# Optimization experiments

Hardware: AMD Instinct MI355X
Metric: run time of the kernel (lower is better)

Reference implementation:

```python
import jax, jax.numpy as jnp
import numpy as np

N, D_IN, D_EMB, K = 16384, 1024, 256, 1024
ALPHA, EPS = 0.01, 1e-5


def setup_inputs() -> dict:
    key = jax.random.key(0)
    ks = jax.random.split(key, 6)
    inp = jax.random.normal(ks[0], (N, D_IN), dtype=jnp.float32)
    W_send = jax.random.normal(ks[1], (D_IN, D_EMB), dtype=jnp.float32) / np.sqrt(D_IN)
    b_send = jnp.zeros((D_EMB,), dtype=jnp.float32)
    W_recv = jax.random.normal(ks[2], (D_EMB, D_IN), dtype=jnp.float32) / np.sqrt(D_EMB)
    b_recv = jnp.zeros((D_IN,), dtype=jnp.float32)
    codebook = jax.random.normal(ks[3], (K, D_EMB), dtype=jnp.float32)
    ema_vecs = codebook.copy()
    ema_size = jnp.zeros((K,), dtype=jnp.float32)
    return {"input": inp, "W_send": W_send, "b_send": b_send,
            "W_recv": W_recv, "b_recv": b_recv, "codebook": codebook,
            "ema_vecs": ema_vecs, "ema_size": ema_size}


def reference(input, W_send, b_send, W_recv, b_recv, codebook, ema_vecs, ema_size):
    sg = jax.lax.stop_gradient
    # send projection -> latent z  [N, D_EMB]
    z = input @ W_send + b_send
    # nearest-neighbor lookup: argmin_k ||e_k||^2 - 2 <z, e_k>
    sqr = jnp.sum(codebook * codebook, axis=1)          # [K]
    cov = jnp.einsum('nj,kj->nk', z, codebook)          # [N, K]
    codes = jnp.argmin(sqr - 2.0 * cov, axis=-1)        # [N] int
    # fetch embeddings (gather)
    vectors = codebook[codes]                            # [N, D_EMB]
    # mse losses, reduction='sum'
    embedding = jnp.sum((vectors - sg(z)) ** 2)
    commitment = jnp.sum((z - sg(vectors)) ** 2)
    # straight-through output
    emb_out = z + sg(vectors - z)
    # EMA accumulate (one-hot scatter == segment_sum)
    upd_vecs = jax.ops.segment_sum(z, codes, num_segments=K)              # [K, D_EMB]
    upd_size = jax.ops.segment_sum(jnp.ones((z.shape[0],), z.dtype), codes, num_segments=K)
    ema_vecs_new = ema_vecs + ALPHA * (upd_vecs - ema_vecs)
    ema_size_new = ema_size + ALPHA * (upd_size - ema_size)
    # EMA update (Laplace-smoothed centroid)
    n = jnp.sum(ema_size_new)
    coef = n / (n + K * EPS)
    size = coef * (ema_size_new + EPS)
    weight_new = ema_vecs_new / size[:, None]
    # empirical entropy of the codes in bits
    prob = jnp.bincount(codes, length=K).astype(jnp.float32) / codes.size
    ent = -jnp.sum(jnp.where(prob > 0, prob * jnp.log(prob), 0.0)) / jnp.log(2.0)
    # recv projection
    x = emb_out @ W_recv + b_recv
    return (x, codes, embedding, commitment, ent, ema_vecs_new, ema_size_new, weight_new)
```

## Files before the change

### kernel.cpp

```cpp
#include <hip/hip_runtime.h>
#include <math.h>

#define NROWS 16384
#define DIN   1024
#define DEMB  256
#define KC    1024
#define ALPHA 0.01f
#define EPSV  1e-5f
#define INV2048 4.8828125e-4f
#define CHUNK 32
#define COV_CHUNKS 8

typedef _Float16 f16;
typedef __attribute__((ext_vector_type(4)))  _Float16 f16x4;
typedef __attribute__((ext_vector_type(8)))  _Float16 f16x8;
typedef __attribute__((ext_vector_type(16))) float    f32x16;
typedef unsigned long long u64;

#define OFF_Z       0
#define OFF_R       4194304
#define OFF_SQR     5242880
#define OFF_ZH      5243904
#define OFF_ZL      7341056
#define OFF_WTH     9438208
#define OFF_WTL     9569280
#define OFF_CBH     9700352
#define OFF_CBL     9831424
#define OFF_KEYS    9962496
#define OFF_CODES   9995264
#define OFF_LIST    10011648
#define OFF_OFFS    10028032
#define OFF_UPD     10029056
#define OFF_HIST    10291200
#define OFF_CURSOR  10292224
#define OFF_LOSS    10293248
#define ZERO_LEN    264208
#define OFF_COUNTSF 10293264
#define OFF_SIZE    10294288

#define OUT_X      0
#define OUT_CODES  16777216
#define OUT_EMB    16793600
#define OUT_COMMIT 16793601
#define OUT_ENT    16793602
#define OUT_EMAV   16793603
#define OUT_EMAS   17055747
#define OUT_W      17056771

__device__ __forceinline__ void split_f32(float x, f16& h, f16& l) {
    h = (f16)x;
    l = (f16)((x - (float)h) * 2048.0f);
}

__global__ __launch_bounds__(64) void sqr_kernel(const float* __restrict__ cb,
                                                 float* __restrict__ sqr) {
    int k = blockIdx.x;
    int lane = threadIdx.x;
    float4 v = ((const float4*)cb)[k * 64 + lane];
    float s = v.x * v.x + v.y * v.y + v.z * v.z + v.w * v.w;
    for (int off = 32; off > 0; off >>= 1) s += __shfl_down(s, off, 64);
    if (lane == 0) sqr[k] = s;
}

__global__ __launch_bounds__(256) void split_wt_kernel(const float* __restrict__ W,
                                                       f16* __restrict__ wth,
                                                       f16* __restrict__ wtl) {
    int n = blockIdx.x;
    int t = threadIdx.x;
    f16x4 h4, l4;
#pragma unroll
    for (int j = 0; j < 4; ++j) {
        int k = t * 4 + j;
        float x = W[(size_t)k * DEMB + n];
        f16 h, l; split_f32(x, h, l);
        h4[j] = h; l4[j] = l;
    }
    *(f16x4*)&wth[(size_t)n * DIN + t * 4] = h4;
    *(f16x4*)&wtl[(size_t)n * DIN + t * 4] = l4;
}

__global__ __launch_bounds__(256) void split_cb_kernel(const float* __restrict__ cb,
                                                       f16* __restrict__ cbh,
                                                       f16* __restrict__ cbl) {
    int idx = (blockIdx.x * 256 + threadIdx.x) * 4;
    float4 v = *(const float4*)&cb[idx];
    f16x4 h4, l4;
    f16 h, l;
    split_f32(v.x, h, l); h4[0] = h; l4[0] = l;
    split_f32(v.y, h, l); h4[1] = h; l4[1] = l;
    split_f32(v.z, h, l); h4[2] = h; l4[2] = l;
    split_f32(v.w, h, l); h4[3] = h; l4[3] = l;
    *(f16x4*)&cbh[idx] = h4;
    *(f16x4*)&cbl[idx] = l4;
}

__global__ __launch_bounds__(128) void gemm1_mfma(const float* __restrict__ in,
                                                  const f16* __restrict__ wth,
                                                  const f16* __restrict__ wtl,
                                                  const float* __restrict__ bsend,
                                                  float* __restrict__ z,
                                                  f16* __restrict__ zh,
                                                  f16* __restrict__ zl) {
    __shared__ f16 sAh[64 * 72], sAl[64 * 72];
    __shared__ f16 sBh[128 * 72], sBl[128 * 72];
    const int tid = threadIdx.x;
    const int wave = tid >> 6, lane = tid & 63;
    const int half = lane >> 5, l31 = lane & 31;
    const int rowBase = blockIdx.y * 64;
    const int colBase = blockIdx.x * 128;

    f32x16 accm[2][2] = {};
    f32x16 accx[2][2] = {};

    const int ar = tid >> 1;
    const int ak = (tid & 1) * 32;

    for (int ks = 0; ks < DIN; ks += 64) {
        __syncthreads();
#pragma unroll
        for (int i = 0; i < 8; ++i) {
            float4 v = *(const float4*)&in[(size_t)(rowBase + ar) * DIN + ks + ak + i * 4];
            f16x4 h4, l4; f16 h, l;
            split_f32(v.x, h, l); h4[0] = h; l4[0] = l;
            split_f32(v.y, h, l); h4[1] = h; l4[1] = l;
            split_f32(v.z, h, l); h4[2] = h; l4[2] = l;
            split_f32(v.w, h, l); h4[3] = h; l4[3] = l;
            *(f16x4*)&sAh[ar * 72 + ak + i * 4] = h4;
            *(f16x4*)&sAl[ar * 72 + ak + i * 4] = l4;
        }
#pragma unroll
        for (int i = 0; i < 8; ++i) {
            f16x8 bh = *(const f16x8*)&wth[(size_t)(colBase + tid) * DIN + ks + i * 8];
            f16x8 bl = *(const f16x8*)&wtl[(size_t)(colBase + tid) * DIN + ks + i * 8];
            *(f16x8*)&sBh[tid * 72 + i * 8] = bh;
            *(f16x8*)&sBl[tid * 72 + i * 8] = bl;
        }
        __syncthreads();
#pragma unroll
        for (int t4 = 0; t4 < 4; ++t4) {
            int seg = t4 * 2 + half;
            f16x8 a_h[2], a_l[2], b_h[2], b_l[2];
#pragma unroll
            for (int rt = 0; rt < 2; ++rt) {
                a_h[rt] = *(const f16x8*)&sAh[(rt * 32 + l31) * 72 + seg * 8];
                a_l[rt] = *(const f16x8*)&sAl[(rt * 32 + l31) * 72 + seg * 8];
            }
#pragma unroll
            for (int ct = 0; ct < 2; ++ct) {
                int nl = wave * 64 + ct * 32 + l31;
                b_h[ct] = *(const f16x8*)&sBh[nl * 72 + seg * 8];
                b_l[ct] = *(const f16x8*)&sBl[nl * 72 + seg * 8];
            }
#pragma unroll
            for (int rt = 0; rt < 2; ++rt)
#pragma unroll
                for (int ct = 0; ct < 2; ++ct) {
                    accm[rt][ct] = __builtin_amdgcn_mfma_f32_32x32x16_f16(
                        a_h[rt], b_h[ct], accm[rt][ct], 0, 0, 0);
                    accx[rt][ct] = __builtin_amdgcn_mfma_f32_32x32x16_f16(
                        a_h[rt], b_l[ct], accx[rt][ct], 0, 0, 0);
                    accx[rt][ct] = __builtin_amdgcn_mfma_f32_32x32x16_f16(
                        a_l[rt], b_h[ct], accx[rt][ct], 0, 0, 0);
                }
        }
    }

#pragma unroll
    for (int rt = 0; rt < 2; ++rt)
#pragma unroll
        for (int ct = 0; ct < 2; ++ct) {
            int col = colBase + wave * 64 + ct * 32 + l31;
            float bb = bsend[col];
#pragma unroll
            for (int reg = 0; reg < 16; ++reg) {
                int row = rowBase + rt * 32 + (reg & 3) + 8 * (reg >> 2) + 4 * half;
                float zv = accm[rt][ct][reg] + INV2048 * accx[rt][ct][reg] + bb;
                size_t o = (size_t)row * DEMB + col;
                z[o] = zv;
                f16 h = (f16)zv;
                zh[o] = h;
                zl[o] = (f16)((zv - (float)h) * 2048.0f);
            }
        }
}

__device__ __forceinline__ void cov_stage(const f16* __restrict__ cbh,
                                          const f16* __restrict__ cbl,
                                          f16* sC, int buf, int codeBase,
                                          int wave, int lane) {
#pragma unroll
    for (int i = 0; i < 8; ++i) {
        const int seg = wave * 8 + i;
        const int hl  = seg >> 4;
        const int rp  = seg & 15;
        const int r   = rp * 2 + (lane >> 5);
        const f16* src = (hl ? cbl : cbh)
                       + (size_t)(codeBase + r) * DEMB
                       + (((lane & 31) ^ r) << 3);
        f16* dst = sC + (((buf << 1) + hl) * 32 + rp * 2) * DEMB;
        __builtin_amdgcn_global_load_lds(
            (const __attribute__((address_space(1))) void*)src,
            (__attribute__((address_space(3))) void*)dst,
            16, 0, 0);
    }
}

__global__ __launch_bounds__(256, 2) void cov_mfma_kernel(const f16* __restrict__ zh,
                                                          const f16* __restrict__ zl,
                                                          const f16* __restrict__ cbh,
                                                          const f16* __restrict__ cbl,
                                                          const float* __restrict__ sqr,
                                                          u64* __restrict__ keys) {
    __shared__ f16 sC[2 * 2 * 32 * DEMB];
    const int tid = threadIdx.x;
    const int wave = tid >> 6, lane = tid & 63;
    const int half = lane >> 5, l31 = lane & 31;
    const int rowBase = blockIdx.y * 128 + wave * 32;
    const int myRow = rowBase + l31;
    const int cb0 = blockIdx.x * (COV_CHUNKS * 32);

    cov_stage(cbh, cbl, sC, 0, cb0, wave, lane);

    f16x8 a_h[16], a_l[16];
#pragma unroll
    for (int t = 0; t < 16; ++t) {
        size_t o = (size_t)myRow * DEMB + t * 16 + half * 8;
        a_h[t] = *(const f16x8*)&zh[o];
        a_l[t] = *(const f16x8*)&zl[o];
    }

    float runv[16];
    int   runc[16];
#pragma unroll
    for (int r = 0; r < 16; ++r) { runv[r] = 3.4e38f; runc[r] = 0; }

    for (int cc = 0; cc < COV_CHUNKS; ++cc) {
        __syncthreads();
        if (cc + 1 < COV_CHUNKS)
            cov_stage(cbh, cbl, sC, (cc + 1) & 1, cb0 + (cc + 1) * 32, wave, lane);

        const f16* Ch = sC + ((cc & 1) * 2 + 0) * 32 * DEMB;
        const f16* Cl = sC + ((cc & 1) * 2 + 1) * 32 * DEMB;

        f32x16 accm = {};
        f32x16 accx = {};
#pragma unroll
        for (int t = 0; t < 16; ++t) {
            const int seg = t * 2 + half;
            const int p = ((seg ^ l31) << 3);
            f16x8 b_h = *(const f16x8*)&Ch[l31 * DEMB + p];
            f16x8 b_l = *(const f16x8*)&Cl[l31 * DEMB + p];
            accm = __builtin_amdgcn_mfma_f32_32x32x16_f16(a_h[t], b_h, accm, 0, 0, 0);
            accx = __builtin_amdgcn_mfma_f32_32x32x16_f16(a_h[t], b_l, accx, 0, 0, 0);
            accx = __builtin_amdgcn_mfma_f32_32x32x16_f16(a_l[t], b_h, accx, 0, 0, 0);
        }

        const int code = cb0 + cc * 32 + l31;
        const float sqv = sqr[code];
#pragma unroll
        for (int r = 0; r < 16; ++r) {
            float s = sqv - 2.0f * (accm[r] + INV2048 * accx[r]);
            if (s < runv[r]) { runv[r] = s; runc[r] = code; }
        }
    }

#pragma unroll
    for (int r = 0; r < 16; ++r) {
        float v = runv[r]; int ci = runc[r];
        for (int off = 16; off > 0; off >>= 1) {
            float ov = __shfl_down(v, off, 32);
            int   oc = __shfl_down(ci, off, 32);
            if (ov < v || (ov == v && oc < ci)) { v = ov; ci = oc; }
        }
        if (l31 == 0) {
            int row = rowBase + (r & 3) + 8 * (r >> 2) + 4 * half;
            unsigned ub = __float_as_uint(v);
            ub = (ub & 0x80000000u) ? ~ub : (ub | 0x80000000u);
            u64 key = ((u64)ub << 32) | (unsigned)ci;
            atomicMin(&keys[row], key);
        }
    }
}

__global__ __launch_bounds__(256) void decode_kernel(const u64* __restrict__ keys,
                                                     int* __restrict__ codes,
                                                     float* __restrict__ out_codes,
                                                     int* __restrict__ hist) {
    int r = blockIdx.x * 256 + threadIdx.x;
    int c = (int)(keys[r] & 0xFFFFFFFFull);
    codes[r] = c;
    out_codes[r] = (float)c;
    atomicAdd(&hist[c], 1);
}

__global__ __launch_bounds__(1024) void prefix_kernel(const int* __restrict__ hist,
                                                      int* __restrict__ offs,
                                                      float* __restrict__ countsf) {
    __shared__ int s[1024];
    int t = threadIdx.x;
    int v = hist[t];
    s[t] = v;
    countsf[t] = (float)v;
    __syncthreads();
    for (int d = 1; d < 1024; d <<= 1) {
        int x = (t >= d) ? s[t - d] : 0;
        __syncthreads();
        s[t] += x;
        __syncthreads();
    }
    offs[t] = s[t] - v;
}

__global__ __launch_bounds__(256) void fill_kernel(const int* __restrict__ codes,
                                                   const int* __restrict__ offs,
                                                   int* __restrict__ cursor,
                                                   int* __restrict__ list) {
    int r = blockIdx.x * 256 + threadIdx.x;
    int c = codes[r];
    int pos = offs[c] + atomicAdd(&cursor[c], 1);
    list[pos] = r;
}

__global__ __launch_bounds__(256) void upd_loss_kernel(const float* __restrict__ z,
                                                       const float* __restrict__ cb,
                                                       const int* __restrict__ list,
                                                       const int* __restrict__ codes,
                                                       float* __restrict__ upd,
                                                       float* __restrict__ loss) {
    __shared__ int srow[CHUNK];
    __shared__ int scode[CHUNK];
    const int tid = threadIdx.x;
    const int base = blockIdx.x * CHUNK;
    if (tid < CHUNK) {
        int r = list[base + tid];
        srow[tid] = r;
        scode[tid] = codes[r];
    }
    __syncthreads();

    int cur = scode[0];
    float cbv = cb[(size_t)cur * DEMB + tid];
    float acc = 0.f, lacc = 0.f;
    float zv = z[(size_t)srow[0] * DEMB + tid];
#pragma unroll 4
    for (int i = 0; i < CHUNK; ++i) {
        float znext = (i + 1 < CHUNK) ? z[(size_t)srow[i + 1] * DEMB + tid] : 0.f;
        int c = scode[i];
        if (c != cur) {
            atomicAdd(&upd[(size_t)cur * DEMB + tid], acc);
            acc = 0.f;
            cur = c;
            cbv = cb[(size_t)cur * DEMB + tid];
        }
        acc += zv;
        float d = zv - cbv;
        lacc += d * d;
        zv = znext;
    }
    atomicAdd(&upd[(size_t)cur * DEMB + tid], acc);

    __shared__ float red[256];
    red[tid] = lacc;
    __syncthreads();
    for (int s = 128; s > 0; s >>= 1) {
        if (tid < s) red[tid] += red[tid + s];
        __syncthreads();
    }
    if (tid == 0) atomicAdd(loss, red[0]);
}

__global__ __launch_bounds__(256) void gemm64_kernel(const float* __restrict__ A,
                                                     const float* __restrict__ B,
                                                     float* __restrict__ C,
                                                     int M, int Kd, int Nc) {
    __shared__ float As[16][68];
    __shared__ float Bs[16][64];
    const int tid = threadIdx.x;
    const int tx = tid & 15, ty = tid >> 4;
    const int rowBase = blockIdx.y * 64;
    const int colBase = blockIdx.x * 64;

    float acc[4][4];
#pragma unroll
    for (int i = 0; i < 4; ++i)
#pragma unroll
        for (int j = 0; j < 4; ++j) acc[i][j] = 0.f;

    const int a_row = tid >> 2;
    const int a_c4  = (tid & 3) * 4;
    const int b_r   = tid >> 4;
    const int b_c4  = (tid & 15) * 4;

    for (int kk = 0; kk < Kd; kk += 16) {
        float4 av = *(const float4*)&A[(size_t)(rowBase + a_row) * Kd + kk + a_c4];
        float4 bv = *(const float4*)&B[(size_t)(kk + b_r) * Nc + colBase + b_c4];
        __syncthreads();
        As[a_c4 + 0][a_row] = av.x;  As[a_c4 + 1][a_row] = av.y;
        As[a_c4 + 2][a_row] = av.z;  As[a_c4 + 3][a_row] = av.w;
        *(float4*)&Bs[b_r][b_c4] = bv;
        __syncthreads();
#pragma unroll
        for (int d = 0; d < 16; ++d) {
            float4 a01 = *(const float4*)&As[d][ty * 4];
            float4 b01 = *(const float4*)&Bs[d][tx * 4];
            float a[4] = {a01.x, a01.y, a01.z, a01.w};
            float b[4] = {b01.x, b01.y, b01.z, b01.w};
#pragma unroll
            for (int i = 0; i < 4; ++i)
#pragma unroll
                for (int j = 0; j < 4; ++j) acc[i][j] += a[i] * b[j];
        }
    }

#pragma unroll
    for (int i = 0; i < 4; ++i) {
        int r = rowBase + ty * 4 + i;
        *(float4*)&C[(size_t)r * Nc + colBase + tx * 4] =
            make_float4(acc[i][0], acc[i][1], acc[i][2], acc[i][3]);
    }
}

__global__ __launch_bounds__(256) void recv_kernel(const float* __restrict__ R,
                                                   const float* __restrict__ brecv,
                                                   const int* __restrict__ codes,
                                                   float* __restrict__ out) {
    const int n = blockIdx.x;
    const int t = threadIdx.x;
    const int code = codes[n];
    float4 r = ((const float4*)(R + (size_t)code * DIN))[t];
    float4 b = ((const float4*)brecv)[t];
    ((float4*)(out + (size_t)n * DIN))[t] =
        make_float4(r.x + b.x, r.y + b.y, r.z + b.z, r.w + b.w);
}

__global__ __launch_bounds__(1024) void ema_small_kernel(const float* __restrict__ ema_size,
                                                         const float* __restrict__ counts,
                                                         const float* __restrict__ loss,
                                                         float* __restrict__ size_ws,
                                                         float* __restrict__ out) {
    __shared__ float rn[1024];
    __shared__ float re[1024];
    const int k = threadIdx.x;
    float c  = counts[k];
    float es = ema_size[k];
    float esn = es + ALPHA * (c - es);
    out[OUT_EMAS + k] = esn;
    float p = c * (1.0f / (float)NROWS);
    rn[k] = esn;
    re[k] = (p > 0.f) ? p * logf(p) : 0.f;
    __syncthreads();
    for (int s = 512; s > 0; s >>= 1) {
        if (k < s) { rn[k] += rn[k + s]; re[k] += re[k + s]; }
        __syncthreads();
    }
    float n = rn[0];
    float coef = n / (n + (float)KC * EPSV);
    size_ws[k] = coef * (esn + EPSV);
    if (k == 0) {
        out[OUT_ENT] = -re[0] / logf(2.0f);
        float l = loss[0];
        out[OUT_EMB] = l;
        out[OUT_COMMIT] = l;
    }
}

__global__ __launch_bounds__(256) void emav_kernel(const float* __restrict__ ema_vecs,
                                                   const float* __restrict__ upd,
                                                   const float* __restrict__ size_ws,
                                                   float* __restrict__ out) {
    int idx = blockIdx.x * 256 + threadIdx.x;
    float ev = ema_vecs[idx], uv = upd[idx];
    float evn = ev + ALPHA * (uv - ev);
    out[OUT_EMAV + idx] = evn;
    out[OUT_W + idx] = evn / size_ws[idx >> 8];
}

extern "C" void kernel_launch(void* const* d_in, const int* in_sizes, int n_in,
                              void* d_out, int out_size, void* d_ws, size_t ws_size,
                              hipStream_t stream) {
    const float* input    = (const float*)d_in[0];
    const float* W_send   = (const float*)d_in[1];
    const float* b_send   = (const float*)d_in[2];
    const float* W_recv   = (const float*)d_in[3];
    const float* b_recv   = (const float*)d_in[4];
    const float* codebook = (const float*)d_in[5];
    const float* ema_vecs = (const float*)d_in[6];
    const float* ema_size = (const float*)d_in[7];
    float* out = (float*)d_out;
    float* ws  = (float*)d_ws;
    int*   wsi = (int*)d_ws;

    f16* wth = (f16*)(ws + OFF_WTH);
    f16* wtl = (f16*)(ws + OFF_WTL);
    f16* cbh = (f16*)(ws + OFF_CBH);
    f16* cbl = (f16*)(ws + OFF_CBL);
    f16* zh  = (f16*)(ws + OFF_ZH);
    f16* zl  = (f16*)(ws + OFF_ZL);
    u64* keys = (u64*)(ws + OFF_KEYS);

    (void)hipMemsetAsync(ws + OFF_UPD, 0, (size_t)ZERO_LEN * sizeof(float), stream);
    (void)hipMemsetAsync(ws + OFF_KEYS, 0xFF, (size_t)NROWS * sizeof(u64), stream);

    sqr_kernel<<<KC, 64, 0, stream>>>(codebook, ws + OFF_SQR);
    split_wt_kernel<<<DEMB, 256, 0, stream>>>(W_send, wth, wtl);
    split_cb_kernel<<<256, 256, 0, stream>>>(codebook, cbh, cbl);

    gemm64_kernel<<<dim3(DIN / 64, KC / 64), 256, 0, stream>>>(
        codebook, W_recv, ws + OFF_R, KC, DEMB, DIN);

    gemm1_mfma<<<dim3(DEMB / 128, NROWS / 64), 128, 0, stream>>>(
        input, wth, wtl, b_send, ws + OFF_Z, zh, zl);

    cov_mfma_kernel<<<dim3(KC / (COV_CHUNKS * 32), NROWS / 128), 256, 0, stream>>>(
        zh, zl, cbh, cbl, ws + OFF_SQR, keys);

    decode_kernel<<<NROWS / 256, 256, 0, stream>>>(
        keys, wsi + OFF_CODES, out + OUT_CODES, wsi + OFF_HIST);

    prefix_kernel<<<1, 1024, 0, stream>>>(
        wsi + OFF_HIST, wsi + OFF_OFFS, ws + OFF_COUNTSF);

    fill_kernel<<<NROWS / 256, 256, 0, stream>>>(
        wsi + OFF_CODES, wsi + OFF_OFFS, wsi + OFF_CURSOR, wsi + OFF_LIST);

    upd_loss_kernel<<<NROWS / CHUNK, 256, 0, stream>>>(
        ws + OFF_Z, codebook, wsi + OFF_LIST, wsi + OFF_CODES,
        ws + OFF_UPD, ws + OFF_LOSS);

    recv_kernel<<<NROWS, 256, 0, stream>>>(
        ws + OFF_R, b_recv, wsi + OFF_CODES, out + OUT_X);

    ema_small_kernel<<<1, 1024, 0, stream>>>(
        ema_size, ws + OFF_COUNTSF, ws + OFF_LOSS, ws + OFF_SIZE, out);

    emav_kernel<<<KC, 256, 0, stream>>>(
        ema_vecs, ws + OFF_UPD, ws + OFF_SIZE, out);
}
```

Baseline: 285.3 us.

## Double-buffer gemm1 with async LDS loads, swizzled layout and 128x128 tiles

Rewrites the first projection GEMM (input @ W_send, split-f16 MFMA) to use 128x128 block tiles with 8 waves instead of 64x128 with 2 waves. The W tiles are now fetched straight into LDS with global_load_lds, and A is prefetched into registers, both double-buffered so global loads overlap the MFMA work. An XOR-swizzled LDS layout replaces the padded one to avoid bank conflicts. The block now needs 128KB of shared memory, which limits occupancy to one block per CU, and the grid shrinks to 256 blocks.

```diff
diff --git a/kernel.cpp b/kernel.cpp
--- a/kernel.cpp
+++ b/kernel.cpp
@@ -94,94 +94,139 @@
     *(f16x4*)&cbl[idx] = l4;
 }
 
-__global__ __launch_bounds__(128) void gemm1_mfma(const float* __restrict__ in,
+__global__ __launch_bounds__(512) void gemm1_mfma(const float* __restrict__ in,
                                                   const f16* __restrict__ wth,
                                                   const f16* __restrict__ wtl,
                                                   const float* __restrict__ bsend,
                                                   float* __restrict__ z,
                                                   f16* __restrict__ zh,
                                                   f16* __restrict__ zl) {
-    __shared__ f16 sAh[64 * 72], sAl[64 * 72];
-    __shared__ f16 sBh[128 * 72], sBl[128 * 72];
+    __shared__ f16 sm[2 * 2 * 2 * 128 * 64];
     const int tid = threadIdx.x;
     const int wave = tid >> 6, lane = tid & 63;
     const int half = lane >> 5, l31 = lane & 31;
-    const int rowBase = blockIdx.y * 64;
+    const int wrow = wave >> 2, wcol = wave & 3;
+    const int rowBase = blockIdx.y * 128;
     const int colBase = blockIdx.x * 128;
 
-    f32x16 accm[2][2] = {};
-    f32x16 accx[2][2] = {};
-
-    const int ar = tid >> 1;
-    const int ak = (tid & 1) * 32;
-
-    for (int ks = 0; ks < DIN; ks += 64) {
-        __syncthreads();
-#pragma unroll
-        for (int i = 0; i < 8; ++i) {
-            float4 v = *(const float4*)&in[(size_t)(rowBase + ar) * DIN + ks + ak + i * 4];
-            f16x4 h4, l4; f16 h, l;
-            split_f32(v.x, h, l); h4[0] = h; l4[0] = l;
-            split_f32(v.y, h, l); h4[1] = h; l4[1] = l;
-            split_f32(v.z, h, l); h4[2] = h; l4[2] = l;
-            split_f32(v.w, h, l); h4[3] = h; l4[3] = l;
-            *(f16x4*)&sAh[ar * 72 + ak + i * 4] = h4;
-            *(f16x4*)&sAl[ar * 72 + ak + i * 4] = l4;
-        }
-#pragma unroll
-        for (int i = 0; i < 8; ++i) {
-            f16x8 bh = *(const f16x8*)&wth[(size_t)(colBase + tid) * DIN + ks + i * 8];
-            f16x8 bl = *(const f16x8*)&wtl[(size_t)(colBase + tid) * DIN + ks + i * 8];
-            *(f16x8*)&sBh[tid * 72 + i * 8] = bh;
-            *(f16x8*)&sBl[tid * 72 + i * 8] = bl;
-        }
-        __syncthreads();
+    const int sr  = tid >> 2;
+    const int skq = tid & 3;
+    const int sr7 = sr & 7;
+
+    f32x16 accm[2] = {};
+    f32x16 accx[2] = {};
+
+    auto stageB = [&](int buf, int ks) {
+#pragma unroll
+        for (int i = 0; i < 4; ++i) {
+            const int q  = wave * 4 + i;
+            const int hl = q >> 4;
+            const int c  = (q & 15) * 8 + (lane >> 3);
+            const int p  = lane & 7;
+            const int s  = p ^ (c & 7);
+            const f16* src = (hl ? wtl : wth)
+                           + (size_t)(colBase + c) * DIN + ks + s * 8;
+            f16* dst = sm + buf * 32768 + 16384 + q * 512 + lane * 8;
+            __builtin_amdgcn_global_load_lds(
+                (const __attribute__((address_space(1))) void*)src,
+                (__attribute__((address_space(3))) void*)dst, 16, 0, 0);
+        }
+    };
+
+    auto loadA = [&](int ks, float4* av) {
+        const float* src = &in[(size_t)(rowBase + sr) * DIN + ks + skq * 16];
+#pragma unroll
+        for (int j = 0; j < 4; ++j) av[j] = ((const float4*)src)[j];
+    };
+
+    auto writeA = [&](int buf, const float4* av) {
+        f16* Abase = sm + buf * 32768;
+#pragma unroll
+        for (int q = 0; q < 2; ++q) {
+            f16x8 h8, l8;
+#pragma unroll
+            for (int j = 0; j < 2; ++j) {
+                float4 v = av[q * 2 + j];
+                f16 h, l;
+                split_f32(v.x, h, l); h8[j * 4 + 0] = h; l8[j * 4 + 0] = l;
+                split_f32(v.y, h, l); h8[j * 4 + 1] = h; l8[j * 4 + 1] = l;
+                split_f32(v.z, h, l); h8[j * 4 + 2] = h; l8[j * 4 + 2] = l;
+                split_f32(v.w, h, l); h8[j * 4 + 3] = h; l8[j * 4 + 3] = l;
+            }
+            const int s = skq * 2 + q;
+            const int off = sr * 64 + ((s ^ sr7) << 3);
+            *(f16x8*)&Abase[off] = h8;
+            *(f16x8*)&Abase[8192 + off] = l8;
+        }
+    };
+
+    auto compute = [&](int buf) {
+        const f16* Ah = sm + buf * 32768;
+        const f16* Al = Ah + 8192;
+        const f16* Bh = Ah + 16384;
+        const f16* Bl = Ah + 24576;
+        const int c  = wcol * 32 + l31;
+        const int c7 = c & 7;
 #pragma unroll
         for (int t4 = 0; t4 < 4; ++t4) {
-            int seg = t4 * 2 + half;
-            f16x8 a_h[2], a_l[2], b_h[2], b_l[2];
+            const int s = t4 * 2 + half;
+            f16x8 a_h[2], a_l[2];
 #pragma unroll
             for (int rt = 0; rt < 2; ++rt) {
-                a_h[rt] = *(const f16x8*)&sAh[(rt * 32 + l31) * 72 + seg * 8];
-                a_l[rt] = *(const f16x8*)&sAl[(rt * 32 + l31) * 72 + seg * 8];
+                const int r = wrow * 64 + rt * 32 + l31;
+                const int off = r * 64 + ((s ^ (r & 7)) << 3);
+                a_h[rt] = *(const f16x8*)&Ah[off];
+                a_l[rt] = *(const f16x8*)&Al[off];
             }
-#pragma unroll
-            for (int ct = 0; ct < 2; ++ct) {
-                int nl = wave * 64 + ct * 32 + l31;
-                b_h[ct] = *(const f16x8*)&sBh[nl * 72 + seg * 8];
-                b_l[ct] = *(const f16x8*)&sBl[nl * 72 + seg * 8];
+            const int boff = c * 64 + ((s ^ c7) << 3);
+            f16x8 b_h = *(const f16x8*)&Bh[boff];
+            f16x8 b_l = *(const f16x8*)&Bl[boff];
+#pragma unroll
+            for (int rt = 0; rt < 2; ++rt) {
+                accm[rt] = __builtin_amdgcn_mfma_f32_32x32x16_f16(a_h[rt], b_h, accm[rt], 0, 0, 0);
+                accx[rt] = __builtin_amdgcn_mfma_f32_32x32x16_f16(a_h[rt], b_l, accx[rt], 0, 0, 0);
+                accx[rt] = __builtin_amdgcn_mfma_f32_32x32x16_f16(a_l[rt], b_h, accx[rt], 0, 0, 0);
             }
-#pragma unroll
-            for (int rt = 0; rt < 2; ++rt)
-#pragma unroll
-                for (int ct = 0; ct < 2; ++ct) {
-                    accm[rt][ct] = __builtin_amdgcn_mfma_f32_32x32x16_f16(
-                        a_h[rt], b_h[ct], accm[rt][ct], 0, 0, 0);
-                    accx[rt][ct] = __builtin_amdgcn_mfma_f32_32x32x16_f16(
-                        a_h[rt], b_l[ct], accx[rt][ct], 0, 0, 0);
-                    accx[rt][ct] = __builtin_amdgcn_mfma_f32_32x32x16_f16(
-                        a_l[rt], b_h[ct], accx[rt][ct], 0, 0, 0);
-                }
-        }
-    }
-
-#pragma unroll
-    for (int rt = 0; rt < 2; ++rt)
-#pragma unroll
-        for (int ct = 0; ct < 2; ++ct) {
-            int col = colBase + wave * 64 + ct * 32 + l31;
-            float bb = bsend[col];
-#pragma unroll
-            for (int reg = 0; reg < 16; ++reg) {
-                int row = rowBase + rt * 32 + (reg & 3) + 8 * (reg >> 2) + 4 * half;
-                float zv = accm[rt][ct][reg] + INV2048 * accx[rt][ct][reg] + bb;
-                size_t o = (size_t)row * DEMB + col;
-                z[o] = zv;
-                f16 h = (f16)zv;
-                zh[o] = h;
-                zl[o] = (f16)((zv - (float)h) * 2048.0f);
-            }
-        }
+        }
+    };
+
+    stageB(0, 0);
+    {
+        float4 av[4];
+        loadA(0, av);
+        writeA(0, av);
+    }
+    __syncthreads();
+
+    int cur = 0;
+    for (int step = 0; step < 16; ++step) {
+        float4 av[4];
+        const bool pf = (step + 1) < 16;
+        if (pf) {
+            stageB(cur ^ 1, (step + 1) * 64);
+            loadA((step + 1) * 64, av);
+        }
+        compute(cur);
+        if (pf) writeA(cur ^ 1, av);
+        __syncthreads();
+        cur ^= 1;
+    }
+
+#pragma unroll
+    for (int rt = 0; rt < 2; ++rt) {
+        const int col = colBase + wcol * 32 + l31;
+        const float bb = bsend[col];
+#pragma unroll
+        for (int reg = 0; reg < 16; ++reg) {
+            const int row = rowBase + wrow * 64 + rt * 32 + (reg & 3) + 8 * (reg >> 2) + 4 * half;
+            const float zv = accm[rt][reg] + INV2048 * accx[rt][reg] + bb;
+            const size_t o = (size_t)row * DEMB + col;
+            z[o] = zv;
+            f16 h = (f16)zv;
+            zh[o] = h;
+            zl[o] = (f16)((zv - (float)h) * 2048.0f);
+        }
+    }
 }
 
 __device__ __forceinline__ void cov_stage(const f16* __restrict__ cbh,
@@ -508,7 +553,7 @@
     gemm64_kernel<<<dim3(DIN / 64, KC / 64), 256, 0, stream>>>(
         codebook, W_recv, ws + OFF_R, KC, DEMB, DIN);
 
-    gemm1_mfma<<<dim3(DEMB / 128, NROWS / 64), 128, 0, stream>>>(
+    gemm1_mfma<<<dim3(DEMB / 128, NROWS / 128), 512, 0, stream>>>(
         input, wth, wtl, b_send, ws + OFF_Z, zh, zl);
 
     cov_mfma_kernel<<<dim3(KC / (COV_CHUNKS * 32), NROWS / 128), 256, 0, stream>>>(
```

Result: faster. 277.3 us (-2.8%).

## Retile send GEMM to 64x64 blocks with XOR-swizzled LDS and direct global-to-LDS loads

Applied to the files above, without the earlier changes.

The send-projection GEMM moves from 64x128 tiles with 2 waves each owning a 2x2 set of MFMA tiles to 64x64 tiles with 4 waves each owning one 32x32 tile, which doubles the grid and raises occupancy (launch bounds 256,4). The split weight tiles are now loaded with global_load_lds straight into shared memory, and all LDS tiles use an XOR swizzle in place of padding to avoid bank conflicts. In exchange, each block reuses loaded data less: the input rows are now read and split twice as often across the column blocks, and there is less MFMA work per LDS fetch.

```diff
diff --git a/kernel.cpp b/kernel.cpp
--- a/kernel.cpp
+++ b/kernel.cpp
@@ -94,94 +94,118 @@
     *(f16x4*)&cbl[idx] = l4;
 }
 
-__global__ __launch_bounds__(128) void gemm1_mfma(const float* __restrict__ in,
-                                                  const f16* __restrict__ wth,
-                                                  const f16* __restrict__ wtl,
-                                                  const float* __restrict__ bsend,
-                                                  float* __restrict__ z,
-                                                  f16* __restrict__ zh,
-                                                  f16* __restrict__ zl) {
-    __shared__ f16 sAh[64 * 72], sAl[64 * 72];
-    __shared__ f16 sBh[128 * 72], sBl[128 * 72];
+__global__ __launch_bounds__(256, 4) void gemm1_mfma(const float* __restrict__ in,
+                                                     const f16* __restrict__ wth,
+                                                     const f16* __restrict__ wtl,
+                                                     const float* __restrict__ bsend,
+                                                     float* __restrict__ z,
+                                                     f16* __restrict__ zh,
+                                                     f16* __restrict__ zl) {
+    __shared__ f16 sm[16384];
     const int tid = threadIdx.x;
     const int wave = tid >> 6, lane = tid & 63;
     const int half = lane >> 5, l31 = lane & 31;
+    const int wr = wave >> 1, wc = wave & 1;
     const int rowBase = blockIdx.y * 64;
-    const int colBase = blockIdx.x * 128;
-
-    f32x16 accm[2][2] = {};
-    f32x16 accx[2][2] = {};
-
-    const int ar = tid >> 1;
-    const int ak = (tid & 1) * 32;
-
-    for (int ks = 0; ks < DIN; ks += 64) {
-        __syncthreads();
-#pragma unroll
-        for (int i = 0; i < 8; ++i) {
-            float4 v = *(const float4*)&in[(size_t)(rowBase + ar) * DIN + ks + ak + i * 4];
-            f16x4 h4, l4; f16 h, l;
-            split_f32(v.x, h, l); h4[0] = h; l4[0] = l;
-            split_f32(v.y, h, l); h4[1] = h; l4[1] = l;
-            split_f32(v.z, h, l); h4[2] = h; l4[2] = l;
-            split_f32(v.w, h, l); h4[3] = h; l4[3] = l;
-            *(f16x4*)&sAh[ar * 72 + ak + i * 4] = h4;
-            *(f16x4*)&sAl[ar * 72 + ak + i * 4] = l4;
-        }
-#pragma unroll
-        for (int i = 0; i < 8; ++i) {
-            f16x8 bh = *(const f16x8*)&wth[(size_t)(colBase + tid) * DIN + ks + i * 8];
-            f16x8 bl = *(const f16x8*)&wtl[(size_t)(colBase + tid) * DIN + ks + i * 8];
-            *(f16x8*)&sBh[tid * 72 + i * 8] = bh;
-            *(f16x8*)&sBl[tid * 72 + i * 8] = bl;
-        }
-        __syncthreads();
-#pragma unroll
-        for (int t4 = 0; t4 < 4; ++t4) {
-            int seg = t4 * 2 + half;
-            f16x8 a_h[2], a_l[2], b_h[2], b_l[2];
-#pragma unroll
-            for (int rt = 0; rt < 2; ++rt) {
-                a_h[rt] = *(const f16x8*)&sAh[(rt * 32 + l31) * 72 + seg * 8];
-                a_l[rt] = *(const f16x8*)&sAl[(rt * 32 + l31) * 72 + seg * 8];
+    const int colBase = blockIdx.x * 64;
+
+    const int sr  = tid >> 2;
+    const int skq = tid & 3;
+    const int sr7 = sr & 7;
+
+    f32x16 accm = {};
+    f32x16 accx = {};
+
+    for (int step = 0; step < 16; ++step) {
+        const int ks = step * 64;
+
+#pragma unroll
+        for (int i = 0; i < 4; ++i) {
+            const int q  = wave * 4 + i;
+            const int hl = q >> 3;
+            const int cq = (q & 7) * 8;
+            const int col = cq + (lane >> 3);
+            const int p  = lane & 7;
+            const int s  = p ^ (col & 7);
+            const f16* src = (hl ? wtl : wth)
+                           + (size_t)(colBase + col) * DIN + ks + s * 8;
+            f16* dst = sm + 8192 + hl * 4096 + cq * 64;
+            __builtin_amdgcn_global_load_lds(
+                (const __attribute__((address_space(1))) void*)src,
+                (__attribute__((address_space(3))) void*)dst, 16, 0, 0);
+        }
+
+        {
+            const float* srcp = &in[(size_t)(rowBase + sr) * DIN + ks + skq * 16];
+            float4 av0 = ((const float4*)srcp)[0];
+            float4 av1 = ((const float4*)srcp)[1];
+            float4 av2 = ((const float4*)srcp)[2];
+            float4 av3 = ((const float4*)srcp)[3];
+            f16 h, l;
+            f16x8 h8, l8;
+            split_f32(av0.x, h, l); h8[0] = h; l8[0] = l;
+            split_f32(av0.y, h, l); h8[1] = h; l8[1] = l;
+            split_f32(av0.z, h, l); h8[2] = h; l8[2] = l;
+            split_f32(av0.w, h, l); h8[3] = h; l8[3] = l;
+            split_f32(av1.x, h, l); h8[4] = h; l8[4] = l;
+            split_f32(av1.y, h, l); h8[5] = h; l8[5] = l;
+            split_f32(av1.z, h, l); h8[6] = h; l8[6] = l;
+            split_f32(av1.w, h, l); h8[7] = h; l8[7] = l;
+            const int o0 = sr * 64 + (((2 * skq + 0) ^ sr7) << 3);
+            *(f16x8*)&sm[o0] = h8;
+            *(f16x8*)&sm[4096 + o0] = l8;
+
+            split_f32(av2.x, h, l); h8[0] = h; l8[0] = l;
+            split_f32(av2.y, h, l); h8[1] = h; l8[1] = l;
+            split_f32(av2.z, h, l); h8[2] = h; l8[2] = l;
+            split_f32(av2.w, h, l); h8[3] = h; l8[3] = l;
+            split_f32(av3.x, h, l); h8[4] = h; l8[4] = l;
+            split_f32(av3.y, h, l); h8[5] = h; l8[5] = l;
+            split_f32(av3.z, h, l); h8[6] = h; l8[6] = l;
+            split_f32(av3.w, h, l); h8[7] = h; l8[7] = l;
+            const int o1 = sr * 64 + (((2 * skq + 1) ^ sr7) << 3);
+            *(f16x8*)&sm[o1] = h8;
+            *(f16x8*)&sm[4096 + o1] = l8;
+        }
+
+        __syncthreads();
+
+        {
+            const int r = wr * 32 + l31;
+            const int c = wc * 32 + l31;
+            const int r7 = r & 7, c7 = c & 7;
+#pragma unroll
+            for (int t = 0; t < 4; ++t) {
+                const int sgi = t * 2 + half;
+                const int aoff = r * 64 + ((sgi ^ r7) << 3);
+                const int boff = c * 64 + ((sgi ^ c7) << 3);
+                f16x8 a_h = *(const f16x8*)&sm[aoff];
+                f16x8 a_l = *(const f16x8*)&sm[4096 + aoff];
+                f16x8 b_h = *(const f16x8*)&sm[8192 + boff];
+                f16x8 b_l = *(const f16x8*)&sm[12288 + boff];
+                accm = __builtin_amdgcn_mfma_f32_32x32x16_f16(a_h, b_h, accm, 0, 0, 0);
+                accx = __builtin_amdgcn_mfma_f32_32x32x16_f16(a_h, b_l, accx, 0, 0, 0);
+                accx = __builtin_amdgcn_mfma_f32_32x32x16_f16(a_l, b_h, accx, 0, 0, 0);
             }
-#pragma unroll
-            for (int ct = 0; ct < 2; ++ct) {
-                int nl = wave * 64 + ct * 32 + l31;
-                b_h[ct] = *(const f16x8*)&sBh[nl * 72 + seg * 8];
-                b_l[ct] = *(const f16x8*)&sBl[nl * 72 + seg * 8];
-            }
-#pragma unroll
-            for (int rt = 0; rt < 2; ++rt)
-#pragma unroll
-                for (int ct = 0; ct < 2; ++ct) {
-                    accm[rt][ct] = __builtin_amdgcn_mfma_f32_32x32x16_f16(
-                        a_h[rt], b_h[ct], accm[rt][ct], 0, 0, 0);
-                    accx[rt][ct] = __builtin_amdgcn_mfma_f32_32x32x16_f16(
-                        a_h[rt], b_l[ct], accx[rt][ct], 0, 0, 0);
-                    accx[rt][ct] = __builtin_amdgcn_mfma_f32_32x32x16_f16(
-                        a_l[rt], b_h[ct], accx[rt][ct], 0, 0, 0);
-                }
-        }
-    }
-
-#pragma unroll
-    for (int rt = 0; rt < 2; ++rt)
-#pragma unroll
-        for (int ct = 0; ct < 2; ++ct) {
-            int col = colBase + wave * 64 + ct * 32 + l31;
-            float bb = bsend[col];
-#pragma unroll
-            for (int reg = 0; reg < 16; ++reg) {
-                int row = rowBase + rt * 32 + (reg & 3) + 8 * (reg >> 2) + 4 * half;
-                float zv = accm[rt][ct][reg] + INV2048 * accx[rt][ct][reg] + bb;
-                size_t o = (size_t)row * DEMB + col;
-                z[o] = zv;
-                f16 h = (f16)zv;
-                zh[o] = h;
-                zl[o] = (f16)((zv - (float)h) * 2048.0f);
-            }
-        }
+        }
+
+        __syncthreads();
+    }
+
+    {
+        const int col = colBase + wc * 32 + l31;
+        const float bb = bsend[col];
+#pragma unroll
+        for (int reg = 0; reg < 16; ++reg) {
+            const int row = rowBase + wr * 32 + (reg & 3) + 8 * (reg >> 2) + 4 * half;
+            const float zv = accm[reg] + INV2048 * accx[reg] + bb;
+            const size_t o = (size_t)row * DEMB + col;
+            z[o] = zv;
+            f16 h = (f16)zv;
+            zh[o] = h;
+            zl[o] = (f16)((zv - (float)h) * 2048.0f);
+        }
+    }
 }
 
 __device__ __forceinline__ void cov_stage(const f16* __restrict__ cbh,
@@ -508,7 +532,7 @@
     gemm64_kernel<<<dim3(DIN / 64, KC / 64), 256, 0, stream>>>(
         codebook, W_recv, ws + OFF_R, KC, DEMB, DIN);
 
-    gemm1_mfma<<<dim3(DEMB / 128, NROWS / 64), 128, 0, stream>>>(
+    gemm1_mfma<<<dim3(DEMB / 64, NROWS / 64), 256, 0, stream>>>(
         input, wth, wtl, b_send, ws + OFF_Z, zh, zl);
 
     cov_mfma_kernel<<<dim3(KC / (COV_CHUNKS * 32), NROWS / 128), 256, 0, stream>>>(
```

Measured after the change: 296.2 us. 1.04x slower.
